# Optimization experiments

Measured on AMD Instinct MI355X. Metric: run time of the kernel, lower is better.

## Reference

```python
import jax, jax.numpy as jnp
import numpy as np

NUM_HEADS = 16
HEAD_DIM = 64


def setup_inputs() -> dict:
    key = jax.random.key(0)
    ks = jax.random.split(key, 6)
    B, S, E = 4, 1024, 1024
    return {
        "x": jax.random.normal(ks[0], (B, S, E), dtype=jnp.float32),
        "W_qkv": jax.random.normal(ks[1], (E, 3 * E), dtype=jnp.float32) * 0.02,
        "b_qkv": jax.random.normal(ks[2], (3 * E,), dtype=jnp.float32) * 0.02,
        "pe": jax.random.normal(ks[3], (S, S, HEAD_DIM), dtype=jnp.float32) * 0.02,
        "W_out": jax.random.normal(ks[4], (E, E), dtype=jnp.float32) * 0.02,
        "b_out": jax.random.normal(ks[5], (E,), dtype=jnp.float32) * 0.02,
    }


def reference(x, W_qkv, b_qkv, pe, W_out, b_out):
    B, S, E = x.shape
    H, D = NUM_HEADS, HEAD_DIM
    scale = D ** -0.5
    # qkv projection: (B,S,3E) -> (3,B,H,S,D)
    qkv = (x @ W_qkv + b_qkv).reshape(B, S, 3, H, D).transpose(2, 0, 3, 1, 4)
    q, k, v = qkv[0], qkv[1], qkv[2]
    # raw scaled scores (NO softmax in original module)
    scores = jnp.einsum('bhxd,bhyd->bhxy', q, k) * scale
    # relative position bias: pe is (S,S,D) == (x,y,c); original permutes to (c,x,y)
    # then einsum('cxy,bnxc->bnxy', pe, q) -> equivalent to 'xyc,bhxc->bhxy'
    pe_q = jnp.einsum('xyc,bhxc->bhxy', pe, q) * scale
    attn = (scores + pe_q) @ v                      # (B,H,S,D)
    out = attn.transpose(0, 2, 1, 3).reshape(B, S, E)
    return out @ W_out + b_out
```

## Files before the change

kernel.cpp:

```cpp
#include <hip/hip_runtime.h>
#include <cstdint>
#include <cstddef>


typedef unsigned short u16;
typedef __bf16 bf16x8 __attribute__((ext_vector_type(8)));
typedef float  f32x4  __attribute__((ext_vector_type(4)));
typedef unsigned short u16x8 __attribute__((ext_vector_type(8)));

#define MFMA16(a, b, c) __builtin_amdgcn_mfma_f32_16x16x32_bf16((a), (b), (c), 0, 0, 0)

#define GLOAD16(g, l)                                                        \
    __builtin_amdgcn_global_load_lds(                                        \
        (const __attribute__((address_space(1))) unsigned int*)(g),          \
        (__attribute__((address_space(3))) unsigned int*)(l), 16, 0, 0)

__device__ __forceinline__ u16 f2bf(float f) {
    __bf16 h = (__bf16)f;
    return __builtin_bit_cast(u16, h);
}
__device__ __forceinline__ float bf2f(u16 u) {
    unsigned int x = ((unsigned int)u) << 16;
    return __builtin_bit_cast(float, x);
}
__device__ __forceinline__ u16x8 pack8(float4 a, float4 b) {
    u16x8 v;
    v[0] = f2bf(a.x); v[1] = f2bf(a.y); v[2] = f2bf(a.z); v[3] = f2bf(a.w);
    v[4] = f2bf(b.x); v[5] = f2bf(b.y); v[6] = f2bf(b.z); v[7] = f2bf(b.w);
    return v;
}

__global__ __launch_bounds__(256) void kxconv(const float* __restrict__ in,
                                              u16* __restrict__ out) {
    int i = (blockIdx.x * 256 + threadIdx.x) * 8;
    float4 f0 = *(const float4*)&in[i];
    float4 f1 = *(const float4*)&in[i + 4];
    *(u16x8*)&out[i] = pack8(f0, f1);
}

__global__ __launch_bounds__(256) void kconv_T(const float* __restrict__ in,
                                               u16* __restrict__ out, int R, int C) {
    __shared__ float tile[64][68];
    const int t  = threadIdx.x;
    const int r0 = blockIdx.y * 64, c0 = blockIdx.x * 64;
    const int rr = t >> 4, c4 = t & 15;
    for (int p = 0; p < 4; ++p) {
        int r = rr + p * 16;
        float4 v = *(const float4*)&in[(size_t)(r0 + r) * C + c0 + c4 * 4];
        *(float4*)&tile[r][c4 * 4] = v;
    }
    __syncthreads();
    for (int p = 0; p < 4; ++p) {
        int n = rr + p * 16;
        ushort4 o;
        o.x = f2bf(tile[c4 * 4 + 0][n]);
        o.y = f2bf(tile[c4 * 4 + 1][n]);
        o.z = f2bf(tile[c4 * 4 + 2][n]);
        o.w = f2bf(tile[c4 * 4 + 3][n]);
        *(ushort4*)&out[(size_t)(c0 + n) * R + r0 + c4 * 4] = o;
    }
}

__global__ __launch_bounds__(256, 2) void kgemm_qkv(const u16* __restrict__ A,
                                                    const u16* __restrict__ WT,
                                                    const float* __restrict__ bias,
                                                    u16* __restrict__ qb,
                                                    u16* __restrict__ kb,
                                                    u16* __restrict__ vb) {
    __shared__ u16 a_s[128 * 64];
    __shared__ u16 b_s[128 * 64];
    const int t = threadIdx.x;
    const int m0 = blockIdx.y * 128, n0 = blockIdx.x * 128;
    const int lane = t & 63, w = t >> 6, lm = lane & 15, lq = lane >> 4;
    const int mb = (w >> 1) * 64, nb = (w & 1) * 64;
    const int sr = t >> 3, sc = (t & 7) * 8;

    f32x4 acc[4][4] = {};
    for (int k0 = 0; k0 < 1024; k0 += 64) {
        __syncthreads();
#pragma unroll
        for (int p = 0; p < 4; ++p) {
            GLOAD16(&A [(size_t)(m0 + p * 32 + sr) * 1024 + k0 + sc], &a_s[p * 2048 + t * 8]);
            GLOAD16(&WT[(size_t)(n0 + p * 32 + sr) * 1024 + k0 + sc], &b_s[p * 2048 + t * 8]);
        }
        __syncthreads();
#pragma unroll
        for (int ks = 0; ks < 2; ++ks) {
            bf16x8 af[4], bfr[4];
#pragma unroll
            for (int mt = 0; mt < 4; ++mt)
                af[mt] = *(const bf16x8*)&a_s[(mb + mt * 16 + lm) * 64 + ks * 32 + lq * 8];
#pragma unroll
            for (int nt = 0; nt < 4; ++nt)
                bfr[nt] = *(const bf16x8*)&b_s[(nb + nt * 16 + lm) * 64 + ks * 32 + lq * 8];
#pragma unroll
            for (int mt = 0; mt < 4; ++mt)
#pragma unroll
                for (int nt = 0; nt < 4; ++nt)
                    acc[mt][nt] = MFMA16(af[mt], bfr[nt], acc[mt][nt]);
        }
    }
    for (int nt = 0; nt < 4; ++nt) {
        int col = n0 + nb + nt * 16 + lm;
        float bv = bias[col];
        int which = col >> 10;
        int h = (col >> 6) & 15, d = col & 63;
        u16* dst = (which == 0) ? qb : ((which == 1) ? kb : vb);
        for (int mt = 0; mt < 4; ++mt) {
            for (int i = 0; i < 4; ++i) {
                int row = m0 + mb + mt * 16 + lq * 4 + i;
                int b = row >> 10, s = row & 1023;
                dst[((size_t)((b * 16 + h) * 1024 + s)) * 64 + d] =
                    f2bf(acc[mt][nt][i] + bv);
            }
        }
    }
}

__global__ __launch_bounds__(256) void ktrans_v(const u16* __restrict__ v,
                                                u16* __restrict__ vt) {
    __shared__ u16 tv[64 * 72];
    const int bid = blockIdx.x;
    const int bh = bid >> 4, s0 = (bid & 15) * 64;
    const int t = threadIdx.x;
    const int rr = t >> 3, cc = t & 7;
    for (int p = 0; p < 2; ++p) {
        int s = rr + p * 32;
        *(u16x8*)&tv[s * 72 + cc * 8] =
            *(const u16x8*)&v[(size_t)(bh * 1024 + s0 + s) * 64 + cc * 8];
    }
    __syncthreads();
    for (int p = 0; p < 2; ++p) {
        int d = rr + p * 32;
        u16x8 o;
#pragma unroll
        for (int j = 0; j < 8; ++j) o[j] = tv[(cc * 8 + j) * 72 + d];
        *(u16x8*)&vt[(size_t)(bh * 64 + d) * 1024 + s0 + cc * 8] = o;
    }
}

__global__ __launch_bounds__(256, 2) void kpq(const u16* __restrict__ qb,
                                              const float* __restrict__ pe,
                                              u16* __restrict__ Pq) {
    __shared__ u16 q_s[64 * 64];
    __shared__ u16 pe_s[2][64 * 80];
    __shared__ u16 o_s[2][64 * 72];
    const int x = blockIdx.x;
    const int t = threadIdx.x;
    const int lane = t & 63, w = t >> 6, lm = lane & 15, lq = lane >> 4;
#pragma unroll
    for (int p = 0; p < 2; ++p)
        GLOAD16(&qb[(size_t)((p * 32 + (t >> 3)) * 1024 + x) * 64 + (t & 7) * 8],
                &q_s[p * 2048 + t * 8]);
    const int yl = t >> 2, cq = (t & 3) * 16;
    const float* pex = pe + (size_t)x * 65536;
    float4 r0, r1, r2, r3;
    {
        const float* src = &pex[(size_t)yl * 64 + cq];
        r0 = *(const float4*)&src[0];  r1 = *(const float4*)&src[4];
        r2 = *(const float4*)&src[8];  r3 = *(const float4*)&src[12];
    }
    int cur = 0;
    const int obh = t >> 2, oyc = t & 3;
    for (int it = 0; it < 16; ++it) {
        *(u16x8*)&pe_s[cur][yl * 80 + cq]     = pack8(r0, r1);
        *(u16x8*)&pe_s[cur][yl * 80 + cq + 8] = pack8(r2, r3);
        __syncthreads();
        if (it < 15) {
            const float* src = &pex[(size_t)((it + 1) * 64 + yl) * 64 + cq];
            r0 = *(const float4*)&src[0];  r1 = *(const float4*)&src[4];
            r2 = *(const float4*)&src[8];  r3 = *(const float4*)&src[12];
        }
        f32x4 acc[4] = {};
#pragma unroll
        for (int ks = 0; ks < 2; ++ks) {
            bf16x8 a = *(const bf16x8*)&pe_s[cur][(16 * w + lm) * 80 + ks * 32 + lq * 8];
#pragma unroll
            for (int nt = 0; nt < 4; ++nt) {
                bf16x8 b = *(const bf16x8*)&q_s[(nt * 16 + lm) * 64 + ks * 32 + lq * 8];
                acc[nt] = MFMA16(a, b, acc[nt]);
            }
        }
#pragma unroll
        for (int nt = 0; nt < 4; ++nt) {
            ushort4 o;
            o.x = f2bf(acc[nt][0]); o.y = f2bf(acc[nt][1]);
            o.z = f2bf(acc[nt][2]); o.w = f2bf(acc[nt][3]);
            *(ushort4*)&o_s[cur][(nt * 16 + lm) * 72 + 16 * w + lq * 4] = o;
        }
        __syncthreads();
        {
            u16x8 a0 = *(const u16x8*)&o_s[cur][obh * 72 + oyc * 16];
            u16x8 a1 = *(const u16x8*)&o_s[cur][obh * 72 + oyc * 16 + 8];
            size_t base = ((size_t)obh * 1024 + x) * 1024 + it * 64 + oyc * 16;
            *(u16x8*)&Pq[base]     = a0;
            *(u16x8*)&Pq[base + 8] = a1;
        }
        cur ^= 1;
    }
}

__global__ __launch_bounds__(256, 2) void kattn(const u16* __restrict__ qb,
                                                const u16* __restrict__ kb,
                                                const u16* __restrict__ vt,
                                                const u16* __restrict__ Pq,
                                                u16* __restrict__ attnb) {
    __shared__ u16 q_s[128 * 64];
    __shared__ u16 k_s[64 * 64];
    __shared__ u16 v_s[64 * 64];
    __shared__ u16 s_s[128 * 80];
    const int bid = blockIdx.x;
    const int bh = bid >> 3, x0 = (bid & 7) * 128;
    const int t = threadIdx.x;
    const int lane = t & 63, w = t >> 6, lm = lane & 15, lq = lane >> 4;
    const int sr = t >> 3, sc = (t & 7) * 8;

#pragma unroll
    for (int p = 0; p < 4; ++p)
        GLOAD16(&qb[(size_t)(bh * 1024 + x0 + p * 32 + sr) * 64 + sc],
                &q_s[p * 2048 + t * 8]);

    const u16* PqRow = Pq + ((size_t)(bh * 1024) + x0 + 32 * w + lm) * 1024 + lq * 4;
    f32x4 oacc[2][4] = {};
    for (int y0 = 0; y0 < 1024; y0 += 64) {
        ushort4 pqr[4][2];
#pragma unroll
        for (int nt = 0; nt < 2; ++nt)
#pragma unroll
            for (int mt = 0; mt < 4; ++mt)
                pqr[mt][nt] = *(const ushort4*)&PqRow[(size_t)(nt * 16) * 1024 + y0 + mt * 16];
        __syncthreads();
#pragma unroll
        for (int p = 0; p < 2; ++p) {
            GLOAD16(&kb[(size_t)(bh * 1024 + y0 + p * 32 + sr) * 64 + sc],
                    &k_s[p * 2048 + t * 8]);
            GLOAD16(&vt[(size_t)(bh * 64 + p * 32 + sr) * 1024 + y0 + sc],
                    &v_s[p * 2048 + t * 8]);
        }
        __syncthreads();
        f32x4 sacc[4][2] = {};
#pragma unroll
        for (int ks = 0; ks < 2; ++ks) {
            bf16x8 bq[2];
#pragma unroll
            for (int nt = 0; nt < 2; ++nt)
                bq[nt] = *(const bf16x8*)&q_s[(32 * w + nt * 16 + lm) * 64 + ks * 32 + lq * 8];
#pragma unroll
            for (int mt = 0; mt < 4; ++mt) {
                bf16x8 ak = *(const bf16x8*)&k_s[(mt * 16 + lm) * 64 + ks * 32 + lq * 8];
#pragma unroll
                for (int nt = 0; nt < 2; ++nt)
                    sacc[mt][nt] = MFMA16(ak, bq[nt], sacc[mt][nt]);
            }
        }
#pragma unroll
        for (int nt = 0; nt < 2; ++nt) {
            int xl = 32 * w + nt * 16 + lm;
#pragma unroll
            for (int mt = 0; mt < 4; ++mt) {
                ushort4 pq = pqr[mt][nt];
                ushort4 o;
                o.x = f2bf((sacc[mt][nt][0] + bf2f(pq.x)) * 0.125f);
                o.y = f2bf((sacc[mt][nt][1] + bf2f(pq.y)) * 0.125f);
                o.z = f2bf((sacc[mt][nt][2] + bf2f(pq.z)) * 0.125f);
                o.w = f2bf((sacc[mt][nt][3] + bf2f(pq.w)) * 0.125f);
                *(ushort4*)&s_s[xl * 80 + mt * 16 + lq * 4] = o;
            }
        }
#pragma unroll
        for (int ks = 0; ks < 2; ++ks) {
            bf16x8 as[2];
#pragma unroll
            for (int mt = 0; mt < 2; ++mt)
                as[mt] = *(const bf16x8*)&s_s[(32 * w + mt * 16 + lm) * 80 + ks * 32 + lq * 8];
#pragma unroll
            for (int nt = 0; nt < 4; ++nt) {
                bf16x8 bv = *(const bf16x8*)&v_s[(nt * 16 + lm) * 64 + ks * 32 + lq * 8];
#pragma unroll
                for (int mt = 0; mt < 2; ++mt)
                    oacc[mt][nt] = MFMA16(as[mt], bv, oacc[mt][nt]);
            }
        }
    }
    const int b = bh >> 4, h = bh & 15;
    for (int mt = 0; mt < 2; ++mt) {
        for (int nt = 0; nt < 4; ++nt) {
            int d = nt * 16 + lm;
            for (int i = 0; i < 4; ++i) {
                int s = x0 + 32 * w + mt * 16 + lq * 4 + i;
                attnb[((size_t)(b * 1024 + s)) * 1024 + h * 64 + d] = f2bf(oacc[mt][nt][i]);
            }
        }
    }
}

__global__ __launch_bounds__(256, 2) void kgemm_out(const u16* __restrict__ A,
                                                    const u16* __restrict__ WT,
                                                    const float* __restrict__ bias,
                                                    float* __restrict__ out) {
    __shared__ u16 a_s[128 * 64];
    __shared__ u16 b_s[128 * 64];
    const int t = threadIdx.x;
    const int m0 = blockIdx.y * 128, n0 = blockIdx.x * 128;
    const int lane = t & 63, w = t >> 6, lm = lane & 15, lq = lane >> 4;
    const int mb = (w >> 1) * 64, nb = (w & 1) * 64;
    const int sr = t >> 3, sc = (t & 7) * 8;

    f32x4 acc[4][4] = {};
    for (int k0 = 0; k0 < 1024; k0 += 64) {
        __syncthreads();
#pragma unroll
        for (int p = 0; p < 4; ++p) {
            GLOAD16(&A [(size_t)(m0 + p * 32 + sr) * 1024 + k0 + sc], &a_s[p * 2048 + t * 8]);
            GLOAD16(&WT[(size_t)(n0 + p * 32 + sr) * 1024 + k0 + sc], &b_s[p * 2048 + t * 8]);
        }
        __syncthreads();
#pragma unroll
        for (int ks = 0; ks < 2; ++ks) {
            bf16x8 af[4], bfr[4];
#pragma unroll
            for (int mt = 0; mt < 4; ++mt)
                af[mt] = *(const bf16x8*)&a_s[(mb + mt * 16 + lm) * 64 + ks * 32 + lq * 8];
#pragma unroll
            for (int nt = 0; nt < 4; ++nt)
                bfr[nt] = *(const bf16x8*)&b_s[(nb + nt * 16 + lm) * 64 + ks * 32 + lq * 8];
#pragma unroll
            for (int mt = 0; mt < 4; ++mt)
#pragma unroll
                for (int nt = 0; nt < 4; ++nt)
                    acc[mt][nt] = MFMA16(af[mt], bfr[nt], acc[mt][nt]);
        }
    }
    for (int nt = 0; nt < 4; ++nt) {
        int col = n0 + nb + nt * 16 + lm;
        float bv = bias[col];
        for (int mt = 0; mt < 4; ++mt) {
            for (int i = 0; i < 4; ++i) {
                int row = m0 + mb + mt * 16 + lq * 4 + i;
                out[(size_t)row * 1024 + col] = acc[mt][nt][i] + bv;
            }
        }
    }
}

extern "C" void kernel_launch(void* const* d_in, const int* in_sizes, int n_in,
                              void* d_out, int out_size, void* d_ws, size_t ws_size,
                              hipStream_t stream) {
    (void)in_sizes; (void)n_in; (void)out_size; (void)ws_size;
    const float* x    = (const float*)d_in[0];
    const float* Wqkv = (const float*)d_in[1];
    const float* bqkv = (const float*)d_in[2];
    const float* pe   = (const float*)d_in[3];
    const float* Wout = (const float*)d_in[4];
    const float* bout = (const float*)d_in[5];
    float* out = (float*)d_out;

    char* ws = (char*)d_ws;
    u16* xb    = (u16*)ws;  ws += (size_t)4096 * 1024 * 2;
    u16* wqkvT = (u16*)ws;  ws += (size_t)3072 * 1024 * 2;
    u16* woutT = (u16*)ws;  ws += (size_t)1024 * 1024 * 2;
    u16* qb    = (u16*)ws;  ws += (size_t)64 * 1024 * 64 * 2;
    u16* kb    = (u16*)ws;  ws += (size_t)64 * 1024 * 64 * 2;
    u16* vb    = (u16*)ws;  ws += (size_t)64 * 1024 * 64 * 2;
    u16* vtb   = (u16*)ws;  ws += (size_t)64 * 64 * 1024 * 2;
    u16* attnb = (u16*)ws;  ws += (size_t)4 * 1024 * 1024 * 2;
    u16* pq    = (u16*)ws;  ws += (size_t)64 * 1024 * 1024 * 2;

    kxconv<<<2048, 256, 0, stream>>>(x, xb);
    kconv_T<<<dim3(48, 16), 256, 0, stream>>>(Wqkv, wqkvT, 1024, 3072);
    kconv_T<<<dim3(16, 16), 256, 0, stream>>>(Wout, woutT, 1024, 1024);
    kgemm_qkv<<<dim3(24, 32), 256, 0, stream>>>(xb, wqkvT, bqkv, qb, kb, vb);
    ktrans_v<<<1024, 256, 0, stream>>>(vb, vtb);
    kpq<<<1024, 256, 0, stream>>>(qb, pe, pq);
    kattn<<<512, 256, 0, stream>>>(qb, kb, vtb, pq, attnb);
    kgemm_out<<<dim3(8, 32), 256, 0, stream>>>(attnb, woutT, bout, out);
}
```

Baseline: 543.3 us.

## Store PE-query bias as fp8, fuse prep kernels, write V transposed from GEMM

```diff
diff --git a/kernel.cpp b/kernel.cpp
--- a/kernel.cpp
+++ b/kernel.cpp
@@ -4,6 +4,7 @@
 
 
 typedef unsigned short u16;
+typedef unsigned char  u8;
 typedef __bf16 bf16x8 __attribute__((ext_vector_type(8)));
 typedef float  f32x4  __attribute__((ext_vector_type(4)));
 typedef unsigned short u16x8 __attribute__((ext_vector_type(8)));
@@ -18,10 +19,6 @@
 __device__ __forceinline__ u16 f2bf(float f) {
     __bf16 h = (__bf16)f;
     return __builtin_bit_cast(u16, h);
-}
-__device__ __forceinline__ float bf2f(u16 u) {
-    unsigned int x = ((unsigned int)u) << 16;
-    return __builtin_bit_cast(float, x);
 }
 __device__ __forceinline__ u16x8 pack8(float4 a, float4 b) {
     u16x8 v;
@@ -30,19 +27,11 @@
     return v;
 }
 
-__global__ __launch_bounds__(256) void kxconv(const float* __restrict__ in,
-                                              u16* __restrict__ out) {
-    int i = (blockIdx.x * 256 + threadIdx.x) * 8;
-    float4 f0 = *(const float4*)&in[i];
-    float4 f1 = *(const float4*)&in[i + 4];
-    *(u16x8*)&out[i] = pack8(f0, f1);
-}
-
-__global__ __launch_bounds__(256) void kconv_T(const float* __restrict__ in,
-                                               u16* __restrict__ out, int R, int C) {
-    __shared__ float tile[64][68];
+__device__ __forceinline__ void convT_tile(const float* __restrict__ in,
+                                           u16* __restrict__ out, int R, int C,
+                                           int bx, int by, float (*tile)[68]) {
     const int t  = threadIdx.x;
-    const int r0 = blockIdx.y * 64, c0 = blockIdx.x * 64;
+    const int r0 = by * 64, c0 = bx * 64;
     const int rr = t >> 4, c4 = t & 15;
     for (int p = 0; p < 4; ++p) {
         int r = rr + p * 16;
@@ -61,12 +50,34 @@
     }
 }
 
+__global__ __launch_bounds__(256) void kprep(const float* __restrict__ x,
+                                             u16* __restrict__ xb,
+                                             const float* __restrict__ Wqkv,
+                                             u16* __restrict__ wqkvT,
+                                             const float* __restrict__ Wout,
+                                             u16* __restrict__ woutT) {
+    __shared__ float tile[64][68];
+    const int bid = blockIdx.x;
+    if (bid < 2048) {
+        int i = (bid * 256 + threadIdx.x) * 8;
+        float4 f0 = *(const float4*)&x[i];
+        float4 f1 = *(const float4*)&x[i + 4];
+        *(u16x8*)&xb[i] = pack8(f0, f1);
+    } else if (bid < 2816) {
+        int r = bid - 2048;
+        convT_tile(Wqkv, wqkvT, 1024, 3072, r % 48, r / 48, tile);
+    } else {
+        int r = bid - 2816;
+        convT_tile(Wout, woutT, 1024, 1024, r % 16, r / 16, tile);
+    }
+}
+
 __global__ __launch_bounds__(256, 2) void kgemm_qkv(const u16* __restrict__ A,
                                                     const u16* __restrict__ WT,
                                                     const float* __restrict__ bias,
                                                     u16* __restrict__ qb,
                                                     u16* __restrict__ kb,
-                                                    u16* __restrict__ vb) {
+                                                    u16* __restrict__ vtb) {
     __shared__ u16 a_s[128 * 64];
     __shared__ u16 b_s[128 * 64];
     const int t = threadIdx.x;
@@ -105,46 +116,32 @@
         float bv = bias[col];
         int which = col >> 10;
         int h = (col >> 6) & 15, d = col & 63;
-        u16* dst = (which == 0) ? qb : ((which == 1) ? kb : vb);
         for (int mt = 0; mt < 4; ++mt) {
-            for (int i = 0; i < 4; ++i) {
-                int row = m0 + mb + mt * 16 + lq * 4 + i;
-                int b = row >> 10, s = row & 1023;
-                dst[((size_t)((b * 16 + h) * 1024 + s)) * 64 + d] =
-                    f2bf(acc[mt][nt][i] + bv);
-            }
-        }
-    }
-}
-
-__global__ __launch_bounds__(256) void ktrans_v(const u16* __restrict__ v,
-                                                u16* __restrict__ vt) {
-    __shared__ u16 tv[64 * 72];
-    const int bid = blockIdx.x;
-    const int bh = bid >> 4, s0 = (bid & 15) * 64;
-    const int t = threadIdx.x;
-    const int rr = t >> 3, cc = t & 7;
-    for (int p = 0; p < 2; ++p) {
-        int s = rr + p * 32;
-        *(u16x8*)&tv[s * 72 + cc * 8] =
-            *(const u16x8*)&v[(size_t)(bh * 1024 + s0 + s) * 64 + cc * 8];
-    }
-    __syncthreads();
-    for (int p = 0; p < 2; ++p) {
-        int d = rr + p * 32;
-        u16x8 o;
-#pragma unroll
-        for (int j = 0; j < 8; ++j) o[j] = tv[(cc * 8 + j) * 72 + d];
-        *(u16x8*)&vt[(size_t)(bh * 64 + d) * 1024 + s0 + cc * 8] = o;
-    }
-}
-
-__global__ __launch_bounds__(256, 2) void kpq(const u16* __restrict__ qb,
+            int row0 = m0 + mb + mt * 16 + lq * 4;
+            int b = row0 >> 10, s = row0 & 1023;
+            if (which == 2) {
+                ushort4 o;
+                o.x = f2bf(acc[mt][nt][0] + bv);
+                o.y = f2bf(acc[mt][nt][1] + bv);
+                o.z = f2bf(acc[mt][nt][2] + bv);
+                o.w = f2bf(acc[mt][nt][3] + bv);
+                *(ushort4*)&vtb[((size_t)(b * 16 + h) * 64 + d) * 1024 + s] = o;
+            } else {
+                u16* dst = (which == 0) ? qb : kb;
+                for (int i = 0; i < 4; ++i)
+                    dst[((size_t)((b * 16 + h) * 1024 + s + i)) * 64 + d] =
+                        f2bf(acc[mt][nt][i] + bv);
+            }
+        }
+    }
+}
+
+__global__ __launch_bounds__(256, 4) void kpq(const u16* __restrict__ qb,
                                               const float* __restrict__ pe,
-                                              u16* __restrict__ Pq) {
+                                              u8* __restrict__ Pq) {
     __shared__ u16 q_s[64 * 64];
-    __shared__ u16 pe_s[2][64 * 80];
-    __shared__ u16 o_s[2][64 * 72];
+    __shared__ u16 pe_s[64 * 80];
+    __shared__ unsigned int o_s[64 * 17];
     const int x = blockIdx.x;
     const int t = threadIdx.x;
     const int lane = t & 63, w = t >> 6, lm = lane & 15, lq = lane >> 4;
@@ -160,11 +157,10 @@
         r0 = *(const float4*)&src[0];  r1 = *(const float4*)&src[4];
         r2 = *(const float4*)&src[8];  r3 = *(const float4*)&src[12];
     }
-    int cur = 0;
     const int obh = t >> 2, oyc = t & 3;
     for (int it = 0; it < 16; ++it) {
-        *(u16x8*)&pe_s[cur][yl * 80 + cq]     = pack8(r0, r1);
-        *(u16x8*)&pe_s[cur][yl * 80 + cq + 8] = pack8(r2, r3);
+        *(u16x8*)&pe_s[yl * 80 + cq]     = pack8(r0, r1);
+        *(u16x8*)&pe_s[yl * 80 + cq + 8] = pack8(r2, r3);
         __syncthreads();
         if (it < 15) {
             const float* src = &pex[(size_t)((it + 1) * 64 + yl) * 64 + cq];
@@ -174,7 +170,7 @@
         f32x4 acc[4] = {};
 #pragma unroll
         for (int ks = 0; ks < 2; ++ks) {
-            bf16x8 a = *(const bf16x8*)&pe_s[cur][(16 * w + lm) * 80 + ks * 32 + lq * 8];
+            bf16x8 a = *(const bf16x8*)&pe_s[(16 * w + lm) * 80 + ks * 32 + lq * 8];
 #pragma unroll
             for (int nt = 0; nt < 4; ++nt) {
                 bf16x8 b = *(const bf16x8*)&q_s[(nt * 16 + lm) * 64 + ks * 32 + lq * 8];
@@ -183,34 +179,32 @@
         }
 #pragma unroll
         for (int nt = 0; nt < 4; ++nt) {
-            ushort4 o;
-            o.x = f2bf(acc[nt][0]); o.y = f2bf(acc[nt][1]);
-            o.z = f2bf(acc[nt][2]); o.w = f2bf(acc[nt][3]);
-            *(ushort4*)&o_s[cur][(nt * 16 + lm) * 72 + 16 * w + lq * 4] = o;
-        }
-        __syncthreads();
-        {
-            u16x8 a0 = *(const u16x8*)&o_s[cur][obh * 72 + oyc * 16];
-            u16x8 a1 = *(const u16x8*)&o_s[cur][obh * 72 + oyc * 16 + 8];
-            size_t base = ((size_t)obh * 1024 + x) * 1024 + it * 64 + oyc * 16;
-            *(u16x8*)&Pq[base]     = a0;
-            *(u16x8*)&Pq[base + 8] = a1;
-        }
-        cur ^= 1;
+            unsigned int pw;
+            pw = __builtin_amdgcn_cvt_pk_fp8_f32(acc[nt][0], acc[nt][1], 0u, false);
+            pw = __builtin_amdgcn_cvt_pk_fp8_f32(acc[nt][2], acc[nt][3], pw, true);
+            o_s[(nt * 16 + lm) * 17 + 4 * w + lq] = pw;
+        }
+        __syncthreads();
+        uint4 dv;
+        dv.x = o_s[obh * 17 + oyc * 4 + 0];
+        dv.y = o_s[obh * 17 + oyc * 4 + 1];
+        dv.z = o_s[obh * 17 + oyc * 4 + 2];
+        dv.w = o_s[obh * 17 + oyc * 4 + 3];
+        *(uint4*)&Pq[((size_t)obh * 1024 + x) * 1024 + it * 64 + oyc * 16] = dv;
     }
 }
 
 __global__ __launch_bounds__(256, 2) void kattn(const u16* __restrict__ qb,
                                                 const u16* __restrict__ kb,
                                                 const u16* __restrict__ vt,
-                                                const u16* __restrict__ Pq,
+                                                const u8* __restrict__ Pq,
                                                 u16* __restrict__ attnb) {
     __shared__ u16 q_s[128 * 64];
     __shared__ u16 k_s[64 * 64];
     __shared__ u16 v_s[64 * 64];
     __shared__ u16 s_s[128 * 80];
     const int bid = blockIdx.x;
-    const int bh = bid >> 3, x0 = (bid & 7) * 128;
+    const int bh = bid & 63, x0 = (bid >> 6) * 128;
     const int t = threadIdx.x;
     const int lane = t & 63, w = t >> 6, lm = lane & 15, lq = lane >> 4;
     const int sr = t >> 3, sc = (t & 7) * 8;
@@ -220,15 +214,15 @@
         GLOAD16(&qb[(size_t)(bh * 1024 + x0 + p * 32 + sr) * 64 + sc],
                 &q_s[p * 2048 + t * 8]);
 
-    const u16* PqRow = Pq + ((size_t)(bh * 1024) + x0 + 32 * w + lm) * 1024 + lq * 4;
+    const u8* PqRow = Pq + ((size_t)(bh * 1024) + x0 + 32 * w + lm) * 1024 + lq * 4;
     f32x4 oacc[2][4] = {};
     for (int y0 = 0; y0 < 1024; y0 += 64) {
-        ushort4 pqr[4][2];
+        unsigned int pqr[4][2];
 #pragma unroll
         for (int nt = 0; nt < 2; ++nt)
 #pragma unroll
             for (int mt = 0; mt < 4; ++mt)
-                pqr[mt][nt] = *(const ushort4*)&PqRow[(size_t)(nt * 16) * 1024 + y0 + mt * 16];
+                pqr[mt][nt] = *(const unsigned int*)&PqRow[(size_t)(nt * 16) * 1024 + y0 + mt * 16];
         __syncthreads();
 #pragma unroll
         for (int p = 0; p < 2; ++p) {
@@ -258,12 +252,12 @@
             int xl = 32 * w + nt * 16 + lm;
 #pragma unroll
             for (int mt = 0; mt < 4; ++mt) {
-                ushort4 pq = pqr[mt][nt];
+                unsigned int pw = pqr[mt][nt];
                 ushort4 o;
-                o.x = f2bf((sacc[mt][nt][0] + bf2f(pq.x)) * 0.125f);
-                o.y = f2bf((sacc[mt][nt][1] + bf2f(pq.y)) * 0.125f);
-                o.z = f2bf((sacc[mt][nt][2] + bf2f(pq.z)) * 0.125f);
-                o.w = f2bf((sacc[mt][nt][3] + bf2f(pq.w)) * 0.125f);
+                o.x = f2bf((sacc[mt][nt][0] + __builtin_amdgcn_cvt_f32_fp8(pw, 0)) * 0.125f);
+                o.y = f2bf((sacc[mt][nt][1] + __builtin_amdgcn_cvt_f32_fp8(pw, 1)) * 0.125f);
+                o.z = f2bf((sacc[mt][nt][2] + __builtin_amdgcn_cvt_f32_fp8(pw, 2)) * 0.125f);
+                o.w = f2bf((sacc[mt][nt][3] + __builtin_amdgcn_cvt_f32_fp8(pw, 3)) * 0.125f);
                 *(ushort4*)&s_s[xl * 80 + mt * 16 + lq * 4] = o;
             }
         }
@@ -361,16 +355,12 @@
     u16* woutT = (u16*)ws;  ws += (size_t)1024 * 1024 * 2;
     u16* qb    = (u16*)ws;  ws += (size_t)64 * 1024 * 64 * 2;
     u16* kb    = (u16*)ws;  ws += (size_t)64 * 1024 * 64 * 2;
-    u16* vb    = (u16*)ws;  ws += (size_t)64 * 1024 * 64 * 2;
     u16* vtb   = (u16*)ws;  ws += (size_t)64 * 64 * 1024 * 2;
     u16* attnb = (u16*)ws;  ws += (size_t)4 * 1024 * 1024 * 2;
-    u16* pq    = (u16*)ws;  ws += (size_t)64 * 1024 * 1024 * 2;
-
-    kxconv<<<2048, 256, 0, stream>>>(x, xb);
-    kconv_T<<<dim3(48, 16), 256, 0, stream>>>(Wqkv, wqkvT, 1024, 3072);
-    kconv_T<<<dim3(16, 16), 256, 0, stream>>>(Wout, woutT, 1024, 1024);
-    kgemm_qkv<<<dim3(24, 32), 256, 0, stream>>>(xb, wqkvT, bqkv, qb, kb, vb);
-    ktrans_v<<<1024, 256, 0, stream>>>(vb, vtb);
+    u8*  pq    = (u8*)ws;   ws += (size_t)64 * 1024 * 1024;
+
+    kprep<<<3072, 256, 0, stream>>>(x, xb, Wqkv, wqkvT, Wout, woutT);
+    kgemm_qkv<<<dim3(24, 32), 256, 0, stream>>>(xb, wqkvT, bqkv, qb, kb, vtb);
     kpq<<<1024, 256, 0, stream>>>(qb, pe, pq);
     kattn<<<512, 256, 0, stream>>>(qb, kb, vtb, pq, attnb);
     kgemm_out<<<dim3(8, 32), 256, 0, stream>>>(attnb, woutT, bout, out);
```

New measurement: 530.3 us. -2.4%, faster.
